# Kernel optimization log

Hardware: AMD Instinct MI355X
Metric: run time of the kernel (lower is better)

The kernel has to match this reference:

```python
import jax, jax.numpy as jnp
import numpy as np
from jax import lax

# Heston model constants (from init_kwargs)
N_STEPS = 512
T = 1.0
V0 = 0.235 ** 2
KAPPA = 1.0
THETA = 0.04
SIGMA_V = 2.0
RHO = -0.7
S0 = 100.0
DT = T / N_STEPS
SQRT_DT = DT ** 0.5
RHO_PERP = (1.0 - RHO * RHO) ** 0.5

BATCH = 65536


def setup_inputs() -> dict:
    key = jax.random.key(0)
    k1, k2 = jax.random.split(key)
    Z_vol = jax.random.normal(k1, (BATCH, N_STEPS, 2), dtype=jnp.float32)
    Z_price = jax.random.normal(k2, (BATCH, N_STEPS), dtype=jnp.float32)
    return {"Z_vol": Z_vol, "Z_price": Z_price}


def reference(Z_vol, Z_price):
    dtype = Z_vol.dtype
    batch = Z_price.shape[0]
    dt = jnp.asarray(DT, dtype)
    sqrt_dt = jnp.asarray(SQRT_DT, dtype)

    # time-major noise for scan: [n_steps, batch]
    Zv = jnp.transpose(Z_vol[:, :, 0])
    Zp = jnp.transpose(Z_price)

    def step(V_k, zs):
        zv, zp = zs
        V_pos = jnp.maximum(V_k, 0.0)  # full truncation
        V_next = V_k + KAPPA * (THETA - V_pos) * dt + SIGMA_V * jnp.sqrt(V_pos * dt) * zv
        V_next = jnp.maximum(V_next, 0.0)
        dB = RHO * sqrt_dt * zv + RHO_PERP * sqrt_dt * zp  # correlated Brownian increment
        log_inc = -0.5 * V_pos * dt + jnp.sqrt(V_pos) * dB
        return V_next, (V_next, log_inc)

    V_init = jnp.full((batch,), V0, dtype=dtype)
    _, (V_path, log_incs) = lax.scan(step, V_init, (Zv, Zp))

    # V: [batch, n_steps+1]
    V = jnp.concatenate([V_init[:, None], jnp.transpose(V_path)], axis=1)
    # cumulative log-price, prepend 0
    log_S = jnp.concatenate(
        [jnp.zeros((batch, 1), dtype=dtype), jnp.cumsum(jnp.transpose(log_incs), axis=1)],
        axis=1,
    )
    S = S0 * jnp.exp(log_S)
    return S, V
```

## Files before the change

### kernel.cpp

```cpp
#include <hip/hip_runtime.h>

#define NSTEPS 512
#define BATCH  65536
#define NOUT   (NSTEPS + 1)
#define TILE   64
#define PAD    65

#define C_DT       (1.0f / 512.0f)
#define C_SQRT_DT  0.04419417382415922f
#define C_RHO      (-0.7f)
#define C_RHOPERP  0.7141428428542850f
#define C_V0       0.055225f
#define C_THETA    0.04f
#define C_SIGMAV   2.0f
#define C_S0       100.0f

__global__ __launch_bounds__(64) void heston_paths(
    const float* __restrict__ Zvol,
    const float* __restrict__ Zp,
    float* __restrict__ S,
    float* __restrict__ V)
{
    __shared__ float St[64][PAD];
    __shared__ float Vt[64][PAD];

    const int lane     = threadIdx.x;
    const int pathBase = blockIdx.x * 64;
    const int b        = pathBase + lane;

    const float4* __restrict__ zv4 = (const float4*)(Zvol + (size_t)b * (NSTEPS * 2));
    const float4* __restrict__ zp4 = (const float4*)(Zp   + (size_t)b * NSTEPS);

    float v    = C_V0;
    float logS = 0.0f;

    S[(size_t)b * NOUT] = C_S0;
    V[(size_t)b * NOUT] = C_V0;

    for (int k0 = 0; k0 < NSTEPS; k0 += TILE) {
        #pragma unroll
        for (int kk = 0; kk < TILE; kk += 8) {
            const int k = k0 + kk;
            const int q = k >> 1;
            float4 a0 = zv4[q + 0];
            float4 a1 = zv4[q + 1];
            float4 a2 = zv4[q + 2];
            float4 a3 = zv4[q + 3];
            float4 p0 = zp4[(k >> 2) + 0];
            float4 p1 = zp4[(k >> 2) + 1];

            float zv[8] = {a0.x, a0.z, a1.x, a1.z, a2.x, a2.z, a3.x, a3.z};
            float zp[8] = {p0.x, p0.y, p0.z, p0.w, p1.x, p1.y, p1.z, p1.w};

            #pragma unroll
            for (int j = 0; j < 8; ++j) {
                const float vpos  = fmaxf(v, 0.0f);
                float vnext = v + (C_THETA - vpos) * C_DT
                                + C_SIGMAV * sqrtf(vpos * C_DT) * zv[j];
                vnext = fmaxf(vnext, 0.0f);
                const float dB = C_RHO * C_SQRT_DT * zv[j]
                               + C_RHOPERP * C_SQRT_DT * zp[j];
                logS += -0.5f * vpos * C_DT + sqrtf(vpos) * dB;
                St[lane][kk + j] = C_S0 * __expf(logS);
                Vt[lane][kk + j] = vnext;
                v = vnext;
            }
        }

        asm volatile("s_waitcnt lgkmcnt(0)" ::: "memory");
        __builtin_amdgcn_wave_barrier();

        const size_t outBase = (size_t)pathBase * NOUT + 1 + k0 + lane;
        #pragma unroll 8
        for (int r = 0; r < 64; ++r) {
            S[outBase + (size_t)r * NOUT] = St[r][lane];
            V[outBase + (size_t)r * NOUT] = Vt[r][lane];
        }

        asm volatile("s_waitcnt lgkmcnt(0)" ::: "memory");
        __builtin_amdgcn_wave_barrier();
    }
}

extern "C" void kernel_launch(void* const* d_in, const int* in_sizes, int n_in,
                              void* d_out, int out_size, void* d_ws, size_t ws_size,
                              hipStream_t stream) {
    const float* Zvol = (const float*)d_in[0];
    const float* Zp   = (const float*)d_in[1];
    float* S = (float*)d_out;
    float* V = S + (size_t)BATCH * NOUT;

    heston_paths<<<BATCH / 64, 64, 0, stream>>>(Zvol, Zp, S, V);
}
```

Measured before the change: 626.1 us.

## Split path kernel into producer wave and three consumer store waves

Restructures the kernel into a 256-thread block where wave 0 runs the sequential Heston recurrence and writes log-price and variance tiles into double-buffered LDS. Waves 1-3 transpose those tiles and write them to global memory, computing the exp for S, so output stores overlap the serial compute of the next tile. The producer also prefetches the next chunk of noise into registers one step ahead. The cost is block-wide barriers every tile, a smaller 32-step tile, and more LDS per block.

```diff
diff --git a/kernel.cpp b/kernel.cpp
--- a/kernel.cpp
+++ b/kernel.cpp
@@ -3,8 +3,9 @@
 #define NSTEPS 512
 #define BATCH  65536
 #define NOUT   (NSTEPS + 1)
-#define TILE   64
-#define PAD    65
+#define TILE   32
+#define NTILES (NSTEPS / TILE)
+#define PAD    34
 
 #define C_DT       (1.0f / 512.0f)
 #define C_SQRT_DT  0.04419417382415922f
@@ -15,71 +16,97 @@
 #define C_SIGMAV   2.0f
 #define C_S0       100.0f
 
-__global__ __launch_bounds__(64) void heston_paths(
+__global__ __launch_bounds__(256, 4) void heston_paths_pc(
     const float* __restrict__ Zvol,
     const float* __restrict__ Zp,
     float* __restrict__ S,
     float* __restrict__ V)
 {
-    __shared__ float St[64][PAD];
-    __shared__ float Vt[64][PAD];
+    __shared__ float Lt[2][64][PAD];
+    __shared__ float Vt[2][64][PAD];
 
-    const int lane     = threadIdx.x;
+    const int tid      = threadIdx.x;
+    const int w        = tid >> 6;
+    const int lane     = tid & 63;
     const int pathBase = blockIdx.x * 64;
     const int b        = pathBase + lane;
 
     const float4* __restrict__ zv4 = (const float4*)(Zvol + (size_t)b * (NSTEPS * 2));
     const float4* __restrict__ zp4 = (const float4*)(Zp   + (size_t)b * NSTEPS);
-
     float v    = C_V0;
     float logS = 0.0f;
+    float4 A0, A1, A2, A3, P0, P1;
+    if (w == 0) {
+        A0 = zv4[0]; A1 = zv4[1]; A2 = zv4[2]; A3 = zv4[3];
+        P0 = zp4[0]; P1 = zp4[1];
+    }
 
-    S[(size_t)b * NOUT] = C_S0;
-    V[(size_t)b * NOUT] = C_V0;
+    const int cw     = w - 1;
+    const int c_col  = lane & 31;
+    const int c_row  = lane >> 5;
 
-    for (int k0 = 0; k0 < NSTEPS; k0 += TILE) {
-        #pragma unroll
-        for (int kk = 0; kk < TILE; kk += 8) {
-            const int k = k0 + kk;
-            const int q = k >> 1;
-            float4 a0 = zv4[q + 0];
-            float4 a1 = zv4[q + 1];
-            float4 a2 = zv4[q + 2];
-            float4 a3 = zv4[q + 3];
-            float4 p0 = zp4[(k >> 2) + 0];
-            float4 p1 = zp4[(k >> 2) + 1];
+    if (w == 1) {
+        S[(size_t)b * NOUT] = C_S0;
+        V[(size_t)b * NOUT] = C_V0;
+    }
 
-            float zv[8] = {a0.x, a0.z, a1.x, a1.z, a2.x, a2.z, a3.x, a3.z};
-            float zp[8] = {p0.x, p0.y, p0.z, p0.w, p1.x, p1.y, p1.z, p1.w};
+    auto consume = [&](int tIdx) {
+        const int buf = tIdx & 1;
+        const int k0  = tIdx * TILE;
+        for (int tau = cw; tau < 64; tau += 3) {
+            const int pair = tau & 31;
+            const int r    = pair * 2 + c_row;
+            const size_t idx = (size_t)(pathBase + r) * NOUT + 1 + k0 + c_col;
+            if (tau < 32) S[idx] = C_S0 * __expf(Lt[buf][r][c_col]);
+            else          V[idx] = Vt[buf][r][c_col];
+        }
+    };
 
+    for (int t = 0; t < NTILES; ++t) {
+        if (w == 0) {
+            const int buf = t & 1;
             #pragma unroll
-            for (int j = 0; j < 8; ++j) {
-                const float vpos  = fmaxf(v, 0.0f);
-                float vnext = v + (C_THETA - vpos) * C_DT
-                                + C_SIGMAV * sqrtf(vpos * C_DT) * zv[j];
-                vnext = fmaxf(vnext, 0.0f);
-                const float dB = C_RHO * C_SQRT_DT * zv[j]
-                               + C_RHOPERP * C_SQRT_DT * zp[j];
-                logS += -0.5f * vpos * C_DT + sqrtf(vpos) * dB;
-                St[lane][kk + j] = C_S0 * __expf(logS);
-                Vt[lane][kk + j] = vnext;
-                v = vnext;
+            for (int cc = 0; cc < 4; ++cc) {
+                const int g = t * 4 + cc;
+                const float4 a0 = A0, a1 = A1, a2 = A2, a3 = A3;
+                const float4 p0 = P0, p1 = P1;
+                if (g + 1 < 4 * NTILES) {
+                    const int q = (g + 1) * 4;
+                    A0 = zv4[q + 0]; A1 = zv4[q + 1];
+                    A2 = zv4[q + 2]; A3 = zv4[q + 3];
+                    P0 = zp4[(g + 1) * 2 + 0]; P1 = zp4[(g + 1) * 2 + 1];
+                }
+                const float zv[8] = {a0.x, a0.z, a1.x, a1.z, a2.x, a2.z, a3.x, a3.z};
+                const float zp[8] = {p0.x, p0.y, p0.z, p0.w, p1.x, p1.y, p1.z, p1.w};
+                float lg[8], vn[8];
+                #pragma unroll
+                for (int j = 0; j < 8; ++j) {
+                    const float vpos  = fmaxf(v, 0.0f);
+                    float vnext = v + (C_THETA - vpos) * C_DT
+                                    + C_SIGMAV * sqrtf(vpos * C_DT) * zv[j];
+                    vnext = fmaxf(vnext, 0.0f);
+                    const float dB = C_RHO * C_SQRT_DT * zv[j]
+                                   + C_RHOPERP * C_SQRT_DT * zp[j];
+                    logS += -0.5f * vpos * C_DT + sqrtf(vpos) * dB;
+                    lg[j] = logS;
+                    vn[j] = vnext;
+                    v = vnext;
+                }
+                const int kk = cc * 8;
+                #pragma unroll
+                for (int j = 0; j < 8; j += 2) {
+                    *(float2*)&Lt[buf][lane][kk + j] = make_float2(lg[j], lg[j + 1]);
+                    *(float2*)&Vt[buf][lane][kk + j] = make_float2(vn[j], vn[j + 1]);
+                }
             }
+        } else if (t > 0) {
+            consume(t - 1);
         }
-
         asm volatile("s_waitcnt lgkmcnt(0)" ::: "memory");
-        __builtin_amdgcn_wave_barrier();
-
-        const size_t outBase = (size_t)pathBase * NOUT + 1 + k0 + lane;
-        #pragma unroll 8
-        for (int r = 0; r < 64; ++r) {
-            S[outBase + (size_t)r * NOUT] = St[r][lane];
-            V[outBase + (size_t)r * NOUT] = Vt[r][lane];
-        }
-
-        asm volatile("s_waitcnt lgkmcnt(0)" ::: "memory");
-        __builtin_amdgcn_wave_barrier();
+        __builtin_amdgcn_s_barrier();
+        asm volatile("" ::: "memory");
     }
+    if (w > 0) consume(NTILES - 1);
 }
 
 extern "C" void kernel_launch(void* const* d_in, const int* in_sizes, int n_in,
@@ -90,5 +117,5 @@
     float* S = (float*)d_out;
     float* V = S + (size_t)BATCH * NOUT;
 
-    heston_paths<<<BATCH / 64, 64, 0, stream>>>(Zvol, Zp, S, V);
+    heston_paths_pc<<<BATCH / 64, 256, 0, stream>>>(Zvol, Zp, S, V);
 }
```

Result: slower. 646.4 us (+3.2%).
